# Kernel tuning notes

Hardware: AMD Instinct MI355X
Metric: run time of the kernel (lower is better)

The kernel has to match this reference:

```python
import jax, jax.numpy as jnp
import numpy as np

PAD_IDX = 0


def setup_inputs() -> dict:
    key = jax.random.key(0)
    ks = jax.random.split(key, 6)
    nentries, entry_size, bsize, nemb, vocab = 8000, 32, 64, 256, 50000
    keys = jax.random.randint(ks[0], (nentries,), 0, vocab)
    entries = jax.random.randint(ks[1], (nentries, entry_size), 0, vocab)
    query = jax.random.normal(ks[2], (bsize, nemb), dtype=jnp.float32)
    wordemb = jax.random.normal(ks[3], (vocab, nemb), dtype=jnp.float32)
    qproj_w = jax.random.uniform(ks[4], (nemb, nemb), jnp.float32, -0.1, 0.1)
    qproj_b = jnp.zeros((nemb,), jnp.float32)
    return dict(keys=keys, entries=entries, query=query, wordemb=wordemb,
                qproj_w=qproj_w, qproj_b=qproj_b)


def _embed(ids, wordemb):
    # F.embedding with padding_idx: gathered rows at pad_idx are zeroed
    return wordemb[ids] * (ids != PAD_IDX)[..., None].astype(wordemb.dtype)


def reference(keys, entries, query, wordemb, qproj_w, qproj_b):
    keys_e = _embed(keys, wordemb)       # (m, d)
    ents_e = _embed(entries, wordemb)    # (m, n, d)
    # --- single hop (max_hops = 1) ---
    # value_atten: query attends over the n tokens inside each entry
    vq = query @ qproj_w.T + qproj_b                       # (b, d)
    logits_v = jnp.einsum('ik,mnk->imn', vq, ents_e)       # (b, m, n)
    prob_v = jax.nn.softmax(logits_v, axis=-1)
    ents = jnp.einsum('imn,mnk->imk', prob_v, ents_e)      # (b, m, d)
    # entry_atten: query attends over entries via their keys
    logits_e = jnp.einsum('ik,jk->ij', query, keys_e)      # (b, m)
    prob_e = jax.nn.softmax(logits_e, axis=-1)
    o_k = prob_e @ keys_e                                  # (b, d)
    combined = jnp.einsum('bm,bme->be', prob_e, ents)      # (b, d)
    # return (us[-1], prob_list[-1], combined_entries)
    return o_k, logits_e, combined
```

## Files before the change

### kernel.cpp

```cpp
#include <hip/hip_runtime.h>
#include <math.h>

#define B 64
#define D 256
#define M 8000
#define N 32
#define LG_LD 8000
#define EPB 16
#define NBLK (M / EPB)

typedef unsigned short u16;
typedef __bf16 bf16x8 __attribute__((ext_vector_type(8)));
typedef float fx4 __attribute__((ext_vector_type(4)));

#define STR_E  264
#define STR_P  40

static __device__ __forceinline__ u16 f2bf(float x) {
    unsigned int u = __float_as_uint(x);
    u += 0x7FFFu + ((u >> 16) & 1u);
    return (u16)(u >> 16);
}
static __device__ __forceinline__ float bf2f(u16 h) {
    return __uint_as_float(((unsigned)h) << 16);
}

__global__ __launch_bounds__(256) void k_prep(const int* __restrict__ keys,
                                              const float* __restrict__ emb,
                                              const float* __restrict__ q,
                                              const float* __restrict__ W,
                                              const float* __restrict__ bias,
                                              u16* __restrict__ embb,
                                              u16* __restrict__ qbf,
                                              u16* __restrict__ keb,
                                              u16* __restrict__ vqb) {
    __shared__ float qs[D];
    int t = threadIdx.x, bid = blockIdx.x;
    if (bid < 6250) {
        size_t idx = (size_t)bid * 2048 + (size_t)t * 8;
        float4 v0 = *(const float4*)(emb + idx);
        float4 v1 = *(const float4*)(emb + idx + 4);
        u16 h[8] = {f2bf(v0.x), f2bf(v0.y), f2bf(v0.z), f2bf(v0.w),
                    f2bf(v1.x), f2bf(v1.y), f2bf(v1.z), f2bf(v1.w)};
        *(uint4*)(embb + idx) = *(uint4*)h;
    } else if (bid < 6258) {
        size_t idx = (size_t)(bid - 6250) * 2048 + (size_t)t * 8;
        float4 v0 = *(const float4*)(q + idx);
        float4 v1 = *(const float4*)(q + idx + 4);
        u16 h[8] = {f2bf(v0.x), f2bf(v0.y), f2bf(v0.z), f2bf(v0.w),
                    f2bf(v1.x), f2bf(v1.y), f2bf(v1.z), f2bf(v1.w)};
        *(uint4*)(qbf + idx) = *(uint4*)h;
    } else if (bid < 7258) {
        int c = (bid - 6258) * 256 + t;
        int j = c >> 5, sp = c & 31;
        int id = keys[j];
        const float* rp = emb + (size_t)id * D + sp * 8;
        float4 v0 = *(const float4*)rp;
        float4 v1 = *(const float4*)(rp + 4);
        float msk = (id != 0) ? 1.f : 0.f;
        u16 h[8] = {f2bf(v0.x * msk), f2bf(v0.y * msk), f2bf(v0.z * msk), f2bf(v0.w * msk),
                    f2bf(v1.x * msk), f2bf(v1.y * msk), f2bf(v1.z * msk), f2bf(v1.w * msk)};
        *(uint4*)(keb + (size_t)j * D + sp * 8) = *(uint4*)h;
    } else {
        int b = bid - 7258;
        qs[t] = q[b * D + t];
        __syncthreads();
        const float* wr = W + t * D;
        float acc = bias[t];
#pragma unroll 8
        for (int k = 0; k < D; k += 4) {
            float4 w4 = *(const float4*)(wr + k);
            acc += qs[k] * w4.x + qs[k + 1] * w4.y + qs[k + 2] * w4.z + qs[k + 3] * w4.w;
        }
        vqb[b * D + t] = f2bf(acc);
    }
}

__global__ __launch_bounds__(256, 2) void k_heavy_f(const int* __restrict__ entries,
                                                    const u16* __restrict__ embb,
                                                    const u16* __restrict__ vqb,
                                                    const u16* __restrict__ qbf,
                                                    const u16* __restrict__ keb,
                                                    float* __restrict__ lg,
                                                    u16* __restrict__ numCp,
                                                    u16* __restrict__ numKp,
                                                    float* __restrict__ mLp,
                                                    float* __restrict__ denLp) {
    __shared__ __align__(16) u16 sEu[2][N * STR_E];
    __shared__ __align__(16) u16 sETu[2][64 * 136];
    __shared__ __align__(16) u16 sPu[B * STR_P];
    __shared__ float sw[EPB][B];

    int t = threadIdx.x;
    int lane = t & 63, l = lane & 15, q = lane >> 4, w = t >> 6;
    int b0 = 16 * w;
    int sp = t & 31, n0 = t >> 5;
    int m0 = blockIdx.x * EPB;
    int bb = t & 63, y = t >> 6;

    int idc[4], idn[4];
    uint4 pf[4];
#pragma unroll
    for (int i = 0; i < 4; ++i) idc[i] = entries[m0 * N + n0 + 8 * i];
#pragma unroll
    for (int i = 0; i < 4; ++i)
        pf[i] = *(const uint4*)(embb + (size_t)idc[i] * D + sp * 8);

    fx4 zero4 = {0.f, 0.f, 0.f, 0.f};
    fx4 aL = zero4;
#pragma unroll
    for (int s = 0; s < 8; ++s) {
        bf16x8 a  = *(const bf16x8*)(qbf + (size_t)(b0 + l) * D + 32 * s + 8 * q);
        bf16x8 bq = *(const bf16x8*)(keb + (size_t)(m0 + l) * D + 32 * s + 8 * q);
        aL = __builtin_amdgcn_mfma_f32_16x16x32_bf16(a, bq, aL, 0, 0, 0);
    }
#pragma unroll
    for (int r = 0; r < 4; ++r)
        lg[(size_t)(b0 + 4 * q + r) * LG_LD + m0 + l] = aL[r];

#pragma unroll
    for (int r = 0; r < 4; ++r) {
        float m_ = aL[r];
        m_ = fmaxf(m_, __shfl_xor(m_, 1));
        m_ = fmaxf(m_, __shfl_xor(m_, 2));
        m_ = fmaxf(m_, __shfl_xor(m_, 4));
        m_ = fmaxf(m_, __shfl_xor(m_, 8));
        float wv = __expf(aL[r] - m_);
        sw[l][b0 + 4 * q + r] = wv;
        float d_ = wv;
        d_ += __shfl_xor(d_, 1);
        d_ += __shfl_xor(d_, 2);
        d_ += __shfl_xor(d_, 4);
        d_ += __shfl_xor(d_, 8);
        if (l == 0) {
            mLp[blockIdx.x * B + b0 + 4 * q + r] = m_;
            denLp[blockIdx.x * B + b0 + 4 * q + r] = d_;
        }
    }

    bf16x8 vqf[8];
#pragma unroll
    for (int s = 0; s < 8; ++s)
        vqf[s] = *(const bf16x8*)(vqb + (b0 + l) * D + 32 * s + 8 * q);

    fx4 acc[16];
#pragma unroll
    for (int dt = 0; dt < 16; ++dt) acc[dt] = zero4;

#pragma unroll
    for (int i = 0; i < 4; ++i) {
        if (idc[i] == 0) pf[i] = make_uint4(0u, 0u, 0u, 0u);
        *(uint4*)&sEu[0][(n0 + 8 * i) * STR_E + sp * 8] = pf[i];
    }
#pragma unroll
    for (int j = 0; j < 8; ++j) {
        unsigned a0 = (((unsigned*)&pf[0])[j >> 1] >> ((j & 1) * 16)) & 0xFFFFu;
        unsigned a1 = (((unsigned*)&pf[1])[j >> 1] >> ((j & 1) * 16)) & 0xFFFFu;
        unsigned a2 = (((unsigned*)&pf[2])[j >> 1] >> ((j & 1) * 16)) & 0xFFFFu;
        unsigned a3 = (((unsigned*)&pf[3])[j >> 1] >> ((j & 1) * 16)) & 0xFFFFu;
        uint2 pr = make_uint2(a0 | (a1 << 16), a2 | (a3 << 16));
        int off = (2 * sp + (j >> 2)) * 136 + (n0 >> 1) * 32 + (j & 3) * 8 + (n0 & 1) * 4;
        *(uint2*)&sETu[0][off] = pr;
    }
#pragma unroll
    for (int i = 0; i < 4; ++i) idc[i] = entries[(m0 + 1) * N + n0 + 8 * i];
#pragma unroll
    for (int i = 0; i < 4; ++i)
        pf[i] = *(const uint4*)(embb + (size_t)idc[i] * D + sp * 8);
#pragma unroll
    for (int i = 0; i < 4; ++i) idn[i] = entries[(m0 + 2) * N + n0 + 8 * i];

    int offL = (l >> 2) * 136 + (l & 3) * 8;

#pragma unroll 2
    for (int e = 0; e < EPB; ++e) {
        __syncthreads();
        int nxt = (e + 1) & 1;
        if (e < EPB - 1) {
#pragma unroll
            for (int i = 0; i < 4; ++i) {
                if (idc[i] == 0) pf[i] = make_uint4(0u, 0u, 0u, 0u);
                *(uint4*)&sEu[nxt][(n0 + 8 * i) * STR_E + sp * 8] = pf[i];
            }
#pragma unroll
            for (int j = 0; j < 8; ++j) {
                unsigned a0 = (((unsigned*)&pf[0])[j >> 1] >> ((j & 1) * 16)) & 0xFFFFu;
                unsigned a1 = (((unsigned*)&pf[1])[j >> 1] >> ((j & 1) * 16)) & 0xFFFFu;
                unsigned a2 = (((unsigned*)&pf[2])[j >> 1] >> ((j & 1) * 16)) & 0xFFFFu;
                unsigned a3 = (((unsigned*)&pf[3])[j >> 1] >> ((j & 1) * 16)) & 0xFFFFu;
                uint2 pr = make_uint2(a0 | (a1 << 16), a2 | (a3 << 16));
                int off = (2 * sp + (j >> 2)) * 136 + (n0 >> 1) * 32 + (j & 3) * 8 + (n0 & 1) * 4;
                *(uint2*)&sETu[nxt][off] = pr;
            }
            if (e < EPB - 2) {
#pragma unroll
                for (int i = 0; i < 4; ++i)
                    pf[i] = *(const uint4*)(embb + (size_t)idn[i] * D + sp * 8);
#pragma unroll
                for (int i = 0; i < 4; ++i) idc[i] = idn[i];
                if (e < EPB - 3) {
#pragma unroll
                    for (int i = 0; i < 4; ++i) idn[i] = entries[(m0 + e + 3) * N + n0 + 8 * i];
                }
            }
        }
        int cur = e & 1;
        fx4 accS[2];
        accS[0] = zero4; accS[1] = zero4;
#pragma unroll
        for (int T = 0; T < 2; ++T)
#pragma unroll
            for (int s = 0; s < 8; ++s) {
                bf16x8 ea = *(const bf16x8*)&sEu[cur][(16 * T + l) * STR_E + 32 * s + 8 * q];
                accS[T] = __builtin_amdgcn_mfma_f32_16x16x32_bf16(ea, vqf[s], accS[T], 0, 0, 0);
            }
        float swb = sw[e][b0 + l];
        float mx = -INFINITY;
#pragma unroll
        for (int T = 0; T < 2; ++T)
#pragma unroll
            for (int r = 0; r < 4; ++r) mx = fmaxf(mx, accS[T][r]);
        mx = fmaxf(mx, __shfl_xor(mx, 16));
        mx = fmaxf(mx, __shfl_xor(mx, 32));
        float pe[2][4], sum = 0.f;
#pragma unroll
        for (int T = 0; T < 2; ++T)
#pragma unroll
            for (int r = 0; r < 4; ++r) {
                pe[T][r] = __expf(accS[T][r] - mx);
                sum += pe[T][r];
            }
        sum += __shfl_xor(sum, 16);
        sum += __shfl_xor(sum, 32);
        float sc = swb / sum;
#pragma unroll
        for (int T = 0; T < 2; ++T)
#pragma unroll
            for (int r = 0; r < 4; ++r) {
                int nn = 16 * T + 4 * q + r;
                int slot = 4 * (nn & 7) + (nn >> 3);
                sPu[(b0 + l) * STR_P + slot] = f2bf(pe[T][r] * sc);
            }
        bf16x8 pa = *(const bf16x8*)&sPu[(b0 + l) * STR_P + 8 * q];
#pragma unroll
        for (int dt = 0; dt < 16; ++dt) {
            bf16x8 eb = *(const bf16x8*)&sETu[cur][offL + dt * 544 + q * 32];
            acc[dt] = __builtin_amdgcn_mfma_f32_16x16x32_bf16(pa, eb, acc[dt], 0, 0, 0);
        }
    }

    u16* ncp = numCp + (size_t)blockIdx.x * (B * D);
#pragma unroll
    for (int dt = 0; dt < 16; ++dt)
#pragma unroll
        for (int r = 0; r < 4; ++r)
            ncp[(b0 + 4 * q + r) * D + 16 * dt + l] = f2bf(acc[dt][r]);

    __syncthreads();
    {
        int rp = t >> 5;
        uint4 ka = *(const uint4*)(keb + (size_t)(m0 + rp) * D + sp * 8);
        uint4 kb = *(const uint4*)(keb + (size_t)(m0 + rp + 8) * D + sp * 8);
#pragma unroll
        for (int j = 0; j < 8; ++j) {
            unsigned a0 = (((unsigned*)&ka)[j >> 1] >> ((j & 1) * 16)) & 0xFFFFu;
            unsigned a1 = (((unsigned*)&kb)[j >> 1] >> ((j & 1) * 16)) & 0xFFFFu;
            int d = 8 * sp + j;
            int sl = 2 * rp;
            int off = (d >> 2) * 136 + (sl >> 3) * 32 + (d & 3) * 8 + (sl & 7);
            *(unsigned*)&sETu[0][off] = a0 | (a1 << 16);
        }
#pragma unroll
        for (int i = 0; i < 4; ++i) {
            int m = 4 * i + y;
            int slot = 2 * (m & 7) + (m >> 3);
            sPu[bb * STR_P + slot] = f2bf(sw[m][bb]);
        }
        *(uint2*)&sPu[bb * STR_P + 16 + 4 * y] = make_uint2(0u, 0u);
    }
    __syncthreads();
    fx4 acc2[16];
#pragma unroll
    for (int dt = 0; dt < 16; ++dt) acc2[dt] = zero4;
    {
        bf16x8 pa2 = *(const bf16x8*)&sPu[(b0 + l) * STR_P + 8 * q];
#pragma unroll
        for (int dt = 0; dt < 16; ++dt) {
            bf16x8 eb2 = *(const bf16x8*)&sETu[0][offL + dt * 544 + q * 32];
            acc2[dt] = __builtin_amdgcn_mfma_f32_16x16x32_bf16(pa2, eb2, acc2[dt], 0, 0, 0);
        }
    }
    u16* nkp = numKp + (size_t)blockIdx.x * (B * D);
#pragma unroll
    for (int dt = 0; dt < 16; ++dt)
#pragma unroll
        for (int r = 0; r < 4; ++r)
            nkp[(b0 + 4 * q + r) * D + 16 * dt + l] = f2bf(acc2[dt][r]);
}

__global__ __launch_bounds__(256) void k_comb2(const u16* __restrict__ numCp,
                                               const u16* __restrict__ numKp,
                                               const float* __restrict__ mLp,
                                               const float* __restrict__ denLp,
                                               float* __restrict__ o_k,
                                               float* __restrict__ comb) {
    __shared__ float sscale[NBLK];
    __shared__ float red[256];
    __shared__ float ro[8][32], rc[8][32];
    __shared__ float srden;
    int bid = blockIdx.x;
    int b = bid >> 3, d0 = (bid & 7) * 32;
    int t = threadIdx.x;
    float mx = -INFINITY;
    for (int blk = t; blk < NBLK; blk += 256) mx = fmaxf(mx, mLp[blk * B + b]);
    red[t] = mx;
    __syncthreads();
    for (int s = 128; s > 0; s >>= 1) {
        if (t < s) red[t] = fmaxf(red[t], red[t + s]);
        __syncthreads();
    }
    float Mg = red[0];
    __syncthreads();
    float ds = 0.f;
    for (int blk = t; blk < NBLK; blk += 256) {
        float sc = __expf(mLp[blk * B + b] - Mg);
        sscale[blk] = sc;
        ds += sc * denLp[blk * B + b];
    }
    red[t] = ds;
    __syncthreads();
    for (int s = 128; s > 0; s >>= 1) {
        if (t < s) red[t] += red[t + s];
        __syncthreads();
    }
    if (t == 0) srden = 1.f / red[0];
    __syncthreads();
    int dd = t & 31, s = t >> 5;
    float ao = 0.f, ac = 0.f;
    for (int blk = s; blk < NBLK; blk += 8) {
        float sc = sscale[blk];
        size_t i = (size_t)blk * (B * D) + (size_t)b * D + d0 + dd;
        ao += sc * bf2f(numKp[i]);
        ac += sc * bf2f(numCp[i]);
    }
    ro[s][dd] = ao;
    rc[s][dd] = ac;
    __syncthreads();
    if (t < 32) {
        float so = 0.f, sc2 = 0.f;
#pragma unroll
        for (int k = 0; k < 8; ++k) { so += ro[k][t]; sc2 += rc[k][t]; }
        float rd = srden;
        o_k[b * D + d0 + t] = so * rd;
        comb[b * D + d0 + t] = sc2 * rd;
    }
}


extern "C" void kernel_launch(void* const* d_in, const int* in_sizes, int n_in,
                              void* d_out, int out_size, void* d_ws, size_t ws_size,
                              hipStream_t stream) {
    const int*   keys    = (const int*)d_in[0];
    const int*   entries = (const int*)d_in[1];
    const float* query   = (const float*)d_in[2];
    const float* wordemb = (const float*)d_in[3];
    const float* qproj_w = (const float*)d_in[4];
    const float* qproj_b = (const float*)d_in[5];

    float* out  = (float*)d_out;
    float* o_k  = out;
    float* lg   = out + B * D;
    float* comb = out + B * D + B * M;

    char* wsb = (char*)d_ws;
    u16*   embb  = (u16*)wsb;
    u16*   keb   = (u16*)(wsb + 25600000);
    u16*   qbf   = (u16*)(wsb + 29696000);
    u16*   vqb   = (u16*)(wsb + 29728768);
    u16*   numCp = (u16*)(wsb + 29761536);
    u16*   numKp = (u16*)(wsb + 46145536);
    float* mLp   = (float*)(wsb + 62529536);
    float* denLp = (float*)(wsb + 62657536);

    k_prep<<<7322, 256, 0, stream>>>(keys, wordemb, query, qproj_w, qproj_b,
                                     embb, qbf, keb, vqb);
    k_heavy_f<<<NBLK, 256, 0, stream>>>(entries, embb, vqb, qbf, keb, lg,
                                        numCp, numKp, mLp, denLp);
    k_comb2<<<512, 256, 0, stream>>>(numCp, numKp, mLp, denLp, o_k, comb);
}
```

Measured before the change: 184.9 us.

## Drop full-table bf16 conversion and gather fp32 embedding rows directly in heavy kernel

```diff
diff --git a/kernel.cpp b/kernel.cpp
--- a/kernel.cpp
+++ b/kernel.cpp
@@ -24,45 +24,42 @@
 static __device__ __forceinline__ float bf2f(u16 h) {
     return __uint_as_float(((unsigned)h) << 16);
 }
-
-__global__ __launch_bounds__(256) void k_prep(const int* __restrict__ keys,
-                                              const float* __restrict__ emb,
-                                              const float* __restrict__ q,
-                                              const float* __restrict__ W,
-                                              const float* __restrict__ bias,
-                                              u16* __restrict__ embb,
-                                              u16* __restrict__ qbf,
-                                              u16* __restrict__ keb,
-                                              u16* __restrict__ vqb) {
+static __device__ __forceinline__ uint4 pack8(float4 va, float4 vb, float msk) {
+    unsigned p0 = (unsigned)f2bf(va.x * msk) | ((unsigned)f2bf(va.y * msk) << 16);
+    unsigned p1 = (unsigned)f2bf(va.z * msk) | ((unsigned)f2bf(va.w * msk) << 16);
+    unsigned p2 = (unsigned)f2bf(vb.x * msk) | ((unsigned)f2bf(vb.y * msk) << 16);
+    unsigned p3 = (unsigned)f2bf(vb.z * msk) | ((unsigned)f2bf(vb.w * msk) << 16);
+    return make_uint4(p0, p1, p2, p3);
+}
+
+__global__ __launch_bounds__(256) void k_prep2(const int* __restrict__ keys,
+                                               const float* __restrict__ emb,
+                                               const float* __restrict__ q,
+                                               const float* __restrict__ W,
+                                               const float* __restrict__ bias,
+                                               u16* __restrict__ qbf,
+                                               u16* __restrict__ keb,
+                                               u16* __restrict__ vqb) {
     __shared__ float qs[D];
     int t = threadIdx.x, bid = blockIdx.x;
-    if (bid < 6250) {
-        size_t idx = (size_t)bid * 2048 + (size_t)t * 8;
-        float4 v0 = *(const float4*)(emb + idx);
-        float4 v1 = *(const float4*)(emb + idx + 4);
-        u16 h[8] = {f2bf(v0.x), f2bf(v0.y), f2bf(v0.z), f2bf(v0.w),
-                    f2bf(v1.x), f2bf(v1.y), f2bf(v1.z), f2bf(v1.w)};
-        *(uint4*)(embb + idx) = *(uint4*)h;
-    } else if (bid < 6258) {
-        size_t idx = (size_t)(bid - 6250) * 2048 + (size_t)t * 8;
-        float4 v0 = *(const float4*)(q + idx);
-        float4 v1 = *(const float4*)(q + idx + 4);
-        u16 h[8] = {f2bf(v0.x), f2bf(v0.y), f2bf(v0.z), f2bf(v0.w),
-                    f2bf(v1.x), f2bf(v1.y), f2bf(v1.z), f2bf(v1.w)};
-        *(uint4*)(qbf + idx) = *(uint4*)h;
-    } else if (bid < 7258) {
-        int c = (bid - 6258) * 256 + t;
+    if (bid < 1000) {
+        int c = bid * 256 + t;
         int j = c >> 5, sp = c & 31;
         int id = keys[j];
         const float* rp = emb + (size_t)id * D + sp * 8;
         float4 v0 = *(const float4*)rp;
         float4 v1 = *(const float4*)(rp + 4);
         float msk = (id != 0) ? 1.f : 0.f;
-        u16 h[8] = {f2bf(v0.x * msk), f2bf(v0.y * msk), f2bf(v0.z * msk), f2bf(v0.w * msk),
-                    f2bf(v1.x * msk), f2bf(v1.y * msk), f2bf(v1.z * msk), f2bf(v1.w * msk)};
-        *(uint4*)(keb + (size_t)j * D + sp * 8) = *(uint4*)h;
+        uint4 pk = pack8(v0, v1, msk);
+        *(uint4*)(keb + (size_t)j * D + sp * 8) = pk;
+    } else if (bid < 1008) {
+        size_t idx = (size_t)(bid - 1000) * 2048 + (size_t)t * 8;
+        float4 v0 = *(const float4*)(q + idx);
+        float4 v1 = *(const float4*)(q + idx + 4);
+        uint4 pk = pack8(v0, v1, 1.f);
+        *(uint4*)(qbf + idx) = pk;
     } else {
-        int b = bid - 7258;
+        int b = bid - 1008;
         qs[t] = q[b * D + t];
         __syncthreads();
         const float* wr = W + t * D;
@@ -77,7 +74,7 @@
 }
 
 __global__ __launch_bounds__(256, 2) void k_heavy_f(const int* __restrict__ entries,
-                                                    const u16* __restrict__ embb,
+                                                    const float* __restrict__ emb,
                                                     const u16* __restrict__ vqb,
                                                     const u16* __restrict__ qbf,
                                                     const u16* __restrict__ keb,
@@ -99,12 +96,15 @@
     int bb = t & 63, y = t >> 6;
 
     int idc[4], idn[4];
-    uint4 pf[4];
+    float4 pfF[8];
 #pragma unroll
     for (int i = 0; i < 4; ++i) idc[i] = entries[m0 * N + n0 + 8 * i];
 #pragma unroll
-    for (int i = 0; i < 4; ++i)
-        pf[i] = *(const uint4*)(embb + (size_t)idc[i] * D + sp * 8);
+    for (int i = 0; i < 4; ++i) {
+        const float* rp = emb + (size_t)idc[i] * D + sp * 8;
+        pfF[2 * i]     = *(const float4*)rp;
+        pfF[2 * i + 1] = *(const float4*)(rp + 4);
+    }
 
     fx4 zero4 = {0.f, 0.f, 0.f, 0.f};
     fx4 aL = zero4;
@@ -147,26 +147,33 @@
 #pragma unroll
     for (int dt = 0; dt < 16; ++dt) acc[dt] = zero4;
 
+    {
+        uint4 pk[4];
+#pragma unroll
+        for (int i = 0; i < 4; ++i) {
+            float msk = (idc[i] != 0) ? 1.f : 0.f;
+            pk[i] = pack8(pfF[2 * i], pfF[2 * i + 1], msk);
+            *(uint4*)&sEu[0][(n0 + 8 * i) * STR_E + sp * 8] = pk[i];
+        }
+#pragma unroll
+        for (int j = 0; j < 8; ++j) {
+            unsigned a0 = (((unsigned*)&pk[0])[j >> 1] >> ((j & 1) * 16)) & 0xFFFFu;
+            unsigned a1 = (((unsigned*)&pk[1])[j >> 1] >> ((j & 1) * 16)) & 0xFFFFu;
+            unsigned a2 = (((unsigned*)&pk[2])[j >> 1] >> ((j & 1) * 16)) & 0xFFFFu;
+            unsigned a3 = (((unsigned*)&pk[3])[j >> 1] >> ((j & 1) * 16)) & 0xFFFFu;
+            uint2 pr = make_uint2(a0 | (a1 << 16), a2 | (a3 << 16));
+            int off = (2 * sp + (j >> 2)) * 136 + (n0 >> 1) * 32 + (j & 3) * 8 + (n0 & 1) * 4;
+            *(uint2*)&sETu[0][off] = pr;
+        }
+    }
+#pragma unroll
+    for (int i = 0; i < 4; ++i) idc[i] = entries[(m0 + 1) * N + n0 + 8 * i];
 #pragma unroll
     for (int i = 0; i < 4; ++i) {
-        if (idc[i] == 0) pf[i] = make_uint4(0u, 0u, 0u, 0u);
-        *(uint4*)&sEu[0][(n0 + 8 * i) * STR_E + sp * 8] = pf[i];
-    }
-#pragma unroll
-    for (int j = 0; j < 8; ++j) {
-        unsigned a0 = (((unsigned*)&pf[0])[j >> 1] >> ((j & 1) * 16)) & 0xFFFFu;
-        unsigned a1 = (((unsigned*)&pf[1])[j >> 1] >> ((j & 1) * 16)) & 0xFFFFu;
-        unsigned a2 = (((unsigned*)&pf[2])[j >> 1] >> ((j & 1) * 16)) & 0xFFFFu;
-        unsigned a3 = (((unsigned*)&pf[3])[j >> 1] >> ((j & 1) * 16)) & 0xFFFFu;
-        uint2 pr = make_uint2(a0 | (a1 << 16), a2 | (a3 << 16));
-        int off = (2 * sp + (j >> 2)) * 136 + (n0 >> 1) * 32 + (j & 3) * 8 + (n0 & 1) * 4;
-        *(uint2*)&sETu[0][off] = pr;
-    }
-#pragma unroll
-    for (int i = 0; i < 4; ++i) idc[i] = entries[(m0 + 1) * N + n0 + 8 * i];
-#pragma unroll
-    for (int i = 0; i < 4; ++i)
-        pf[i] = *(const uint4*)(embb + (size_t)idc[i] * D + sp * 8);
+        const float* rp = emb + (size_t)idc[i] * D + sp * 8;
+        pfF[2 * i]     = *(const float4*)rp;
+        pfF[2 * i + 1] = *(const float4*)(rp + 4);
+    }
 #pragma unroll
     for (int i = 0; i < 4; ++i) idn[i] = entries[(m0 + 2) * N + n0 + 8 * i];
 
@@ -177,25 +184,30 @@
         __syncthreads();
         int nxt = (e + 1) & 1;
         if (e < EPB - 1) {
+            uint4 pk[4];
 #pragma unroll
             for (int i = 0; i < 4; ++i) {
-                if (idc[i] == 0) pf[i] = make_uint4(0u, 0u, 0u, 0u);
-                *(uint4*)&sEu[nxt][(n0 + 8 * i) * STR_E + sp * 8] = pf[i];
+                float msk = (idc[i] != 0) ? 1.f : 0.f;
+                pk[i] = pack8(pfF[2 * i], pfF[2 * i + 1], msk);
+                *(uint4*)&sEu[nxt][(n0 + 8 * i) * STR_E + sp * 8] = pk[i];
             }
 #pragma unroll
             for (int j = 0; j < 8; ++j) {
-                unsigned a0 = (((unsigned*)&pf[0])[j >> 1] >> ((j & 1) * 16)) & 0xFFFFu;
-                unsigned a1 = (((unsigned*)&pf[1])[j >> 1] >> ((j & 1) * 16)) & 0xFFFFu;
-                unsigned a2 = (((unsigned*)&pf[2])[j >> 1] >> ((j & 1) * 16)) & 0xFFFFu;
-                unsigned a3 = (((unsigned*)&pf[3])[j >> 1] >> ((j & 1) * 16)) & 0xFFFFu;
+                unsigned a0 = (((unsigned*)&pk[0])[j >> 1] >> ((j & 1) * 16)) & 0xFFFFu;
+                unsigned a1 = (((unsigned*)&pk[1])[j >> 1] >> ((j & 1) * 16)) & 0xFFFFu;
+                unsigned a2 = (((unsigned*)&pk[2])[j >> 1] >> ((j & 1) * 16)) & 0xFFFFu;
+                unsigned a3 = (((unsigned*)&pk[3])[j >> 1] >> ((j & 1) * 16)) & 0xFFFFu;
                 uint2 pr = make_uint2(a0 | (a1 << 16), a2 | (a3 << 16));
                 int off = (2 * sp + (j >> 2)) * 136 + (n0 >> 1) * 32 + (j & 3) * 8 + (n0 & 1) * 4;
                 *(uint2*)&sETu[nxt][off] = pr;
             }
             if (e < EPB - 2) {
 #pragma unroll
-                for (int i = 0; i < 4; ++i)
-                    pf[i] = *(const uint4*)(embb + (size_t)idn[i] * D + sp * 8);
+                for (int i = 0; i < 4; ++i) {
+                    const float* rp = emb + (size_t)idn[i] * D + sp * 8;
+                    pfF[2 * i]     = *(const float4*)rp;
+                    pfF[2 * i + 1] = *(const float4*)(rp + 4);
+                }
 #pragma unroll
                 for (int i = 0; i < 4; ++i) idc[i] = idn[i];
                 if (e < EPB - 3) {
@@ -373,18 +385,17 @@
     float* comb = out + B * D + B * M;
 
     char* wsb = (char*)d_ws;
-    u16*   embb  = (u16*)wsb;
-    u16*   keb   = (u16*)(wsb + 25600000);
-    u16*   qbf   = (u16*)(wsb + 29696000);
-    u16*   vqb   = (u16*)(wsb + 29728768);
-    u16*   numCp = (u16*)(wsb + 29761536);
-    u16*   numKp = (u16*)(wsb + 46145536);
-    float* mLp   = (float*)(wsb + 62529536);
-    float* denLp = (float*)(wsb + 62657536);
-
-    k_prep<<<7322, 256, 0, stream>>>(keys, wordemb, query, qproj_w, qproj_b,
-                                     embb, qbf, keb, vqb);
-    k_heavy_f<<<NBLK, 256, 0, stream>>>(entries, embb, vqb, qbf, keb, lg,
+    u16*   keb   = (u16*)wsb;
+    u16*   qbf   = (u16*)(wsb + 4096000);
+    u16*   vqb   = (u16*)(wsb + 4128768);
+    u16*   numCp = (u16*)(wsb + 4161536);
+    u16*   numKp = (u16*)(wsb + 20545536);
+    float* mLp   = (float*)(wsb + 36929536);
+    float* denLp = (float*)(wsb + 37057536);
+
+    k_prep2<<<1072, 256, 0, stream>>>(keys, wordemb, query, qproj_w, qproj_b,
+                                      qbf, keb, vqb);
+    k_heavy_f<<<NBLK, 256, 0, stream>>>(entries, wordemb, vqb, qbf, keb, lg,
                                         numCp, numKp, mLp, denLp);
     k_comb2<<<512, 256, 0, stream>>>(numCp, numKp, mLp, denLp, o_k, comb);
 }
```

Result: faster. 175.9 us, median of 2 (-4.9%).
